# Kernel tuning notes

Hardware: AMD Instinct MI355X
Metric: run time of the kernel (lower is better)

The kernel has to match this reference:

```python
import jax, jax.numpy as jnp
import numpy as np

NUM_HEAD = 8


def setup_inputs() -> dict:
    key = jax.random.key(0)
    ks = jax.random.split(key, 9)
    B, T, Hz, N, H, Tc = 8, 48, 24, 1024, 512, 64
    return {
        "encoder_hidden": jax.random.normal(ks[0], (B, T, N, H), dtype=jnp.float32),
        "x_time": jax.random.normal(ks[1], (B, T, Tc), dtype=jnp.float32),
        "target_time": jax.random.normal(ks[2], (B, Hz, Tc), dtype=jnp.float32),
        "Wq": jax.random.normal(ks[3], (Tc, H), dtype=jnp.float32) * (Tc ** -0.5),
        "bq": jax.random.normal(ks[4], (H,), dtype=jnp.float32) * 0.02,
        "Wk": jax.random.normal(ks[5], (Tc, H), dtype=jnp.float32) * (Tc ** -0.5),
        "bk": jax.random.normal(ks[6], (H,), dtype=jnp.float32) * 0.02,
        "Wv": jax.random.normal(ks[7], (H, H), dtype=jnp.float32) * (H ** -0.5),
        "bv": jax.random.normal(ks[8], (H,), dtype=jnp.float32) * 0.02,
    }


def reference(encoder_hidden, x_time, target_time, Wq, bq, Wk, bk, Wv, bv):
    # encoder_hidden: [B, T, N, H]; x_time: [B, T, Tc]; target_time: [B, Hz, Tc]
    B, T, N, H = encoder_hidden.shape
    nh = NUM_HEAD
    d = H // nh
    Hz = target_time.shape[1]
    # Linear projections; split/cat over heads == reshape last dim to [nh, d]
    q = (target_time @ Wq + bq).reshape(B, Hz, nh, d)      # [B, Hz, nh, d]
    k = (x_time @ Wk + bk).reshape(B, T, nh, d)            # [B, T, nh, d]
    v = (encoder_hidden @ Wv + bv).reshape(B, T, N, nh, d)  # [B, T, N, nh, d]
    # Attention over time, shared across nodes
    scores = jnp.einsum('bihd,bjhd->bhij', q, k) / (d ** 0.5)  # [B, nh, Hz, T]
    attn = jax.nn.softmax(scores, axis=-1)
    # Broadcast attention across the node dimension
    X = jnp.einsum('bhij,bjnhd->binhd', attn, v)           # [B, Hz, N, nh, d]
    return X.reshape(B, Hz, N, H)                           # [B, Hz, N, H]
```

## Files before the change

### kernel.cpp

```cpp
#include <hip/hip_runtime.h>
#include <hip/hip_bf16.h>

#define Bb 8
#define Tt 48
#define HZ 24
#define Nn 1024
#define Hh 512
#define NHEAD 8

typedef short short8 __attribute__((ext_vector_type(8)));
typedef float f32x4 __attribute__((ext_vector_type(4)));

__device__ __forceinline__ ushort f2bf(float f) {
  uint u = __builtin_bit_cast(uint, f);
  u += 0x7FFFu + ((u >> 16) & 1u);
  return (ushort)(u >> 16);
}

__global__ void wvt2_kernel(const float* __restrict__ Wv, ushort* __restrict__ W2) {
  int t = blockIdx.x * 256 + threadIdx.x;
  int e = t & 7;
  int lane = (t >> 3) & 63;
  int f = (t >> 9) & 3;
  int kb = (t >> 11) & 7;
  int w = (t >> 14) & 3;
  int ch = t >> 16;
  int ki = f >> 1, nn = f & 1;
  int row = ch * 128 + w * 32 + nn * 16 + (lane & 15);
  int col = kb * 64 + ki * 32 + ((lane >> 4) << 3) + e;
  W2[t] = f2bf(Wv[col * 512 + row]);
}

__global__ void attn_kernel(const float* __restrict__ xt, const float* __restrict__ tt,
                            const float* __restrict__ Wq, const float* __restrict__ bq,
                            const float* __restrict__ Wk, const float* __restrict__ bk,
                            ushort* __restrict__ attnp) {
  __shared__ float qs[24][65];
  __shared__ float ks_[48][65];
  __shared__ float sc[24][49];
  int bh = blockIdx.x;
  int b = bh >> 3, h = bh & 7;
  int t = threadIdx.x;
  for (int e = t; e < 24 * 64; e += 256) {
    int i = e >> 6, dd = e & 63;
    float s = bq[h * 64 + dd];
    const float* r = tt + (b * 24 + i) * 64;
    #pragma unroll 8
    for (int c = 0; c < 64; ++c) s += r[c] * Wq[c * 512 + h * 64 + dd];
    qs[i][dd] = s;
  }
  for (int e = t; e < 48 * 64; e += 256) {
    int j = e >> 6, dd = e & 63;
    float s = bk[h * 64 + dd];
    const float* r = xt + (b * 48 + j) * 64;
    #pragma unroll 8
    for (int c = 0; c < 64; ++c) s += r[c] * Wk[c * 512 + h * 64 + dd];
    ks_[j][dd] = s;
  }
  __syncthreads();
  for (int e = t; e < 24 * 48; e += 256) {
    int i = e / 48, j = e - i * 48;
    float s = 0.f;
    #pragma unroll 8
    for (int dd = 0; dd < 64; ++dd) s += qs[i][dd] * ks_[j][dd];
    sc[i][j] = s * 0.125f;
  }
  __syncthreads();
  if (t < 32) {
    int i = t;
    ushort* orow = attnp + ((size_t)bh * 32 + i) * 64;
    if (i < 24) {
      float mx = -1e30f;
      for (int j = 0; j < 48; ++j) mx = fmaxf(mx, sc[i][j]);
      float sum = 0.f;
      for (int j = 0; j < 48; ++j) { float e = expf(sc[i][j] - mx); sc[i][j] = e; sum += e; }
      float inv = 1.f / sum;
      for (int j = 0; j < 48; ++j) orow[j] = f2bf(sc[i][j] * inv);
      for (int j = 48; j < 64; ++j) orow[j] = 0;
    } else {
      for (int j = 0; j < 64; ++j) orow[j] = 0;
    }
  }
}

#define A_BASE 0
#define V_BASE 49152

__global__ __launch_bounds__(256, 2) void main_kernel(
    const float* __restrict__ EH, const ushort* __restrict__ W2,
    const ushort* __restrict__ attnp, const float* __restrict__ bv,
    float* __restrict__ out) {
  __shared__ __align__(128) char smem[65536];
  int bid = blockIdx.x;
  int b = bid >> 10, n = bid & 1023;
  int t = threadIdx.x;
  int lane = t & 63, w = t >> 6;
  int rowl = lane & 15;
  int colb = (lane >> 4) << 3;
  char* vbuf = smem + V_BASE + w * 4096;

  float bvr[4][2];
  #pragma unroll
  for (int c = 0; c < 4; ++c)
    #pragma unroll
    for (int nn = 0; nn < 2; ++nn)
      bvr[c][nn] = bv[c * 128 + w * 32 + nn * 16 + rowl];

  {
    int lr = lane >> 1;
    int off = (lr << 7) + ((96 + ((lane & 1) << 4)) ^ ((lr & 7) << 4));
    *(uint4*)(vbuf + off) = make_uint4(0, 0, 0, 0);
  }

  const ushort* wp0 = W2 + (size_t)w * 16384 + lane * 8;

  short8 bc[4], bn[4];
  #pragma unroll
  for (int f = 0; f < 4; ++f) bc[f] = *(const short8*)(wp0 + f * 512);

  {
    const float* ehb = EH + (((size_t)b * Tt) * Nn + n) * Hh;
    #pragma unroll 8
    for (int it = 0; it < 24; ++it) {
      int f = it * 256 + t;
      int j = f >> 7, c4 = f & 127;
      float4 v = *(const float4*)(ehb + (size_t)j * (Nn * Hh) + c4 * 4);
      uint2 p;
      p.x = (uint)f2bf(v.x) | ((uint)f2bf(v.y) << 16);
      p.y = (uint)f2bf(v.z) | ((uint)f2bf(v.w) << 16);
      int off = (j << 10) + (c4 << 3);
      off ^= (j & 7) << 4;
      *(uint2*)(smem + A_BASE + off) = p;
    }
  }
  __syncthreads();

  #pragma unroll
  for (int ch = 0; ch < 4; ++ch) {
    const ushort* wp = W2 + (size_t)(ch * 4 + w) * 16384 + lane * 8;
    f32x4 acc[3][2] = {};
    #pragma unroll
    for (int kb = 0; kb < 8; ++kb) {
      if (kb < 7) {
        #pragma unroll
        for (int f = 0; f < 4; ++f)
          bn[f] = *(const short8*)(wp + (kb + 1) * 2048 + f * 512);
      } else if (ch < 3) {
        #pragma unroll
        for (int f = 0; f < 4; ++f)
          bn[f] = *(const short8*)(wp + 65536 + f * 512);
      }
      #pragma unroll
      for (int ki = 0; ki < 2; ++ki) {
        short8 af[3];
        int kc = kb * 64 + ki * 32 + colb;
        #pragma unroll
        for (int m = 0; m < 3; ++m) {
          int j = m * 16 + rowl;
          int off = (j << 10) + (kc << 1);
          off ^= (j & 7) << 4;
          af[m] = *(const short8*)(smem + A_BASE + off);
        }
        #pragma unroll
        for (int m = 0; m < 3; ++m) {
          acc[m][0] = __builtin_amdgcn_mfma_f32_16x16x32_bf16(af[m], bc[ki * 2 + 0], acc[m][0], 0, 0, 0);
          acc[m][1] = __builtin_amdgcn_mfma_f32_16x16x32_bf16(af[m], bc[ki * 2 + 1], acc[m][1], 0, 0, 0);
        }
      }
      #pragma unroll
      for (int f = 0; f < 4; ++f) bc[f] = bn[f];
    }

    int h = 2 * ch + (w >> 1);
    short8 pa[2][2];
    #pragma unroll
    for (int ks = 0; ks < 2; ++ks)
      #pragma unroll
      for (int itl = 0; itl < 2; ++itl) {
        int i = itl * 16 + rowl;
        pa[ks][itl] = *(const short8*)(attnp + (((size_t)(b * 8 + h) * 32 + i) * 64) + ks * 32 + colb);
      }

    #pragma unroll
    for (int m = 0; m < 3; ++m) {
      #pragma unroll
      for (int nn = 0; nn < 2; ++nn) {
        int lr = nn * 16 + rowl;
        int j0 = m * 16 + ((lane >> 4) << 2);
        uint2 p;
        p.x = (uint)f2bf(acc[m][nn][0]) | ((uint)f2bf(acc[m][nn][1]) << 16);
        p.y = (uint)f2bf(acc[m][nn][2]) | ((uint)f2bf(acc[m][nn][3]) << 16);
        int off = (lr << 7) + ((j0 << 1) ^ ((lr & 7) << 4));
        *(uint2*)(vbuf + off) = p;
      }
    }
    asm volatile("s_waitcnt lgkmcnt(0)" ::: "memory");
    __builtin_amdgcn_sched_barrier(0);

    f32x4 x[2][2] = {};
    #pragma unroll
    for (int ks = 0; ks < 2; ++ks) {
      short8 vb[2];
      #pragma unroll
      for (int nn = 0; nn < 2; ++nn) {
        int lr = nn * 16 + rowl;
        int off = (lr << 7) + (((ks * 32 + colb) << 1) ^ ((lr & 7) << 4));
        vb[nn] = *(const short8*)(vbuf + off);
      }
      #pragma unroll
      for (int itl = 0; itl < 2; ++itl)
        #pragma unroll
        for (int nn = 0; nn < 2; ++nn)
          x[itl][nn] = __builtin_amdgcn_mfma_f32_16x16x32_bf16(pa[ks][itl], vb[nn], x[itl][nn], 0, 0, 0);
    }

    #pragma unroll
    for (int itl = 0; itl < 2; ++itl) {
      int ib = itl * 16 + ((lane >> 4) << 2);
      #pragma unroll
      for (int nn = 0; nn < 2; ++nn) {
        int hd = ch * 128 + w * 32 + nn * 16 + rowl;
        float bvv = bvr[ch][nn];
        #pragma unroll
        for (int r = 0; r < 4; ++r) {
          int i = ib + r;
          if (i < 24)
            out[(((size_t)b * HZ + i) * Nn + n) * Hh + hd] = x[itl][nn][r] + bvv;
        }
      }
    }
  }
}

extern "C" void kernel_launch(void* const* d_in, const int* in_sizes, int n_in,
                              void* d_out, int out_size, void* d_ws, size_t ws_size,
                              hipStream_t stream) {
  (void)in_sizes; (void)n_in; (void)out_size; (void)ws_size;
  const float* EH = (const float*)d_in[0];
  const float* xt = (const float*)d_in[1];
  const float* tt = (const float*)d_in[2];
  const float* Wq = (const float*)d_in[3];
  const float* bq = (const float*)d_in[4];
  const float* Wk = (const float*)d_in[5];
  const float* bk = (const float*)d_in[6];
  const float* Wv = (const float*)d_in[7];
  const float* bv = (const float*)d_in[8];
  float* out = (float*)d_out;
  ushort* W2 = (ushort*)d_ws;
  ushort* attnp = (ushort*)((char*)d_ws + 512 * 1024);

  wvt2_kernel<<<1024, 256, 0, stream>>>(Wv, W2);
  attn_kernel<<<64, 256, 0, stream>>>(xt, tt, Wq, bq, Wk, bk, attnp);
  main_kernel<<<8192, 256, 0, stream>>>(EH, W2, attnp, bv, out);
}
```

Measured before the change: 468.9 us.

## Stream encoder tile in K chunks overlapped with MFMA, swap loop order

The kernel no longer loads the whole 48x512 encoder slice into shared memory before any compute. It loads two 64-wide K chunks up front, then inside a kb-outer loop it prefetches chunk kb+2 into registers, runs the MFMAs for all four output chunks on chunk kb, and converts and stores the prefetched chunk before a barrier. To make this possible the loop nest is inverted so all four ch accumulators live at once (96 floats per thread), and the Wv fragment prefetch is replaced by direct loads right before use. The aim is to hide global-memory latency behind matrix math. The cost is higher register pressure, a barrier per K step, and unprefetched weight loads.

```diff
diff --git a/kernel.cpp b/kernel.cpp
--- a/kernel.cpp
+++ b/kernel.cpp
@@ -112,65 +112,83 @@
     *(uint4*)(vbuf + off) = make_uint4(0, 0, 0, 0);
   }
 
-  const ushort* wp0 = W2 + (size_t)w * 16384 + lane * 8;
-
-  short8 bc[4], bn[4];
-  #pragma unroll
-  for (int f = 0; f < 4; ++f) bc[f] = *(const short8*)(wp0 + f * 512);
-
-  {
-    const float* ehb = EH + (((size_t)b * Tt) * Nn + n) * Hh;
-    #pragma unroll 8
-    for (int it = 0; it < 24; ++it) {
-      int f = it * 256 + t;
-      int j = f >> 7, c4 = f & 127;
-      float4 v = *(const float4*)(ehb + (size_t)j * (Nn * Hh) + c4 * 4);
+  const float* ehb = EH + (((size_t)b * Tt) * Nn + n) * Hh;
+  int sj = t >> 4, sc4 = t & 15;
+
+  #pragma unroll
+  for (int s = 0; s < 2; ++s) {
+    #pragma unroll
+    for (int i = 0; i < 3; ++i) {
+      int j = sj + i * 16;
+      float4 v = *(const float4*)(ehb + (size_t)j * (Nn * Hh) + (s * 16 + sc4) * 4);
       uint2 p;
       p.x = (uint)f2bf(v.x) | ((uint)f2bf(v.y) << 16);
       p.y = (uint)f2bf(v.z) | ((uint)f2bf(v.w) << 16);
-      int off = (j << 10) + (c4 << 3);
+      int off = (j << 10) + (((s * 16 + sc4)) << 3);
       off ^= (j & 7) << 4;
       *(uint2*)(smem + A_BASE + off) = p;
     }
   }
   __syncthreads();
 
+  f32x4 acc[4][3][2] = {};
+  #pragma unroll
+  for (int kb = 0; kb < 8; ++kb) {
+    float4 ldv[3];
+    if (kb < 6) {
+      #pragma unroll
+      for (int i = 0; i < 3; ++i) {
+        int j = sj + i * 16;
+        ldv[i] = *(const float4*)(ehb + (size_t)j * (Nn * Hh) + ((kb + 2) * 16 + sc4) * 4);
+      }
+    }
+    short8 af[2][3];
+    #pragma unroll
+    for (int ki = 0; ki < 2; ++ki) {
+      int kc = kb * 64 + ki * 32 + colb;
+      #pragma unroll
+      for (int m = 0; m < 3; ++m) {
+        int j = m * 16 + rowl;
+        int off = (j << 10) + (kc << 1);
+        off ^= (j & 7) << 4;
+        af[ki][m] = *(const short8*)(smem + A_BASE + off);
+      }
+    }
+    #pragma unroll
+    for (int ch = 0; ch < 4; ++ch) {
+      const ushort* wpf = W2 + (size_t)(ch * 4 + w) * 16384 + kb * 2048 + lane * 8;
+      short8 bf0 = *(const short8*)(wpf);
+      short8 bf1 = *(const short8*)(wpf + 512);
+      short8 bf2 = *(const short8*)(wpf + 1024);
+      short8 bf3 = *(const short8*)(wpf + 1536);
+      #pragma unroll
+      for (int m = 0; m < 3; ++m) {
+        acc[ch][m][0] = __builtin_amdgcn_mfma_f32_16x16x32_bf16(af[0][m], bf0, acc[ch][m][0], 0, 0, 0);
+        acc[ch][m][1] = __builtin_amdgcn_mfma_f32_16x16x32_bf16(af[0][m], bf1, acc[ch][m][1], 0, 0, 0);
+      }
+      #pragma unroll
+      for (int m = 0; m < 3; ++m) {
+        acc[ch][m][0] = __builtin_amdgcn_mfma_f32_16x16x32_bf16(af[1][m], bf2, acc[ch][m][0], 0, 0, 0);
+        acc[ch][m][1] = __builtin_amdgcn_mfma_f32_16x16x32_bf16(af[1][m], bf3, acc[ch][m][1], 0, 0, 0);
+      }
+    }
+    if (kb < 6) {
+      #pragma unroll
+      for (int i = 0; i < 3; ++i) {
+        int j = sj + i * 16;
+        uint2 p;
+        p.x = (uint)f2bf(ldv[i].x) | ((uint)f2bf(ldv[i].y) << 16);
+        p.y = (uint)f2bf(ldv[i].z) | ((uint)f2bf(ldv[i].w) << 16);
+        int off = (j << 10) + (((kb + 2) * 16 + sc4)) << 3;
+        off = ((j << 10) + (((kb + 2) * 16 + sc4) << 3)) ^ ((j & 7) << 4);
+        *(uint2*)(smem + A_BASE + off) = p;
+      }
+    }
+    __syncthreads();
+  }
+
   #pragma unroll
   for (int ch = 0; ch < 4; ++ch) {
-    const ushort* wp = W2 + (size_t)(ch * 4 + w) * 16384 + lane * 8;
-    f32x4 acc[3][2] = {};
-    #pragma unroll
-    for (int kb = 0; kb < 8; ++kb) {
-      if (kb < 7) {
-        #pragma unroll
-        for (int f = 0; f < 4; ++f)
-          bn[f] = *(const short8*)(wp + (kb + 1) * 2048 + f * 512);
-      } else if (ch < 3) {
-        #pragma unroll
-        for (int f = 0; f < 4; ++f)
-          bn[f] = *(const short8*)(wp + 65536 + f * 512);
-      }
-      #pragma unroll
-      for (int ki = 0; ki < 2; ++ki) {
-        short8 af[3];
-        int kc = kb * 64 + ki * 32 + colb;
-        #pragma unroll
-        for (int m = 0; m < 3; ++m) {
-          int j = m * 16 + rowl;
-          int off = (j << 10) + (kc << 1);
-          off ^= (j & 7) << 4;
-          af[m] = *(const short8*)(smem + A_BASE + off);
-        }
-        #pragma unroll
-        for (int m = 0; m < 3; ++m) {
-          acc[m][0] = __builtin_amdgcn_mfma_f32_16x16x32_bf16(af[m], bc[ki * 2 + 0], acc[m][0], 0, 0, 0);
-          acc[m][1] = __builtin_amdgcn_mfma_f32_16x16x32_bf16(af[m], bc[ki * 2 + 1], acc[m][1], 0, 0, 0);
-        }
-      }
-      #pragma unroll
-      for (int f = 0; f < 4; ++f) bc[f] = bn[f];
-    }
-
     int h = 2 * ch + (w >> 1);
     short8 pa[2][2];
     #pragma unroll
@@ -188,8 +206,8 @@
         int lr = nn * 16 + rowl;
         int j0 = m * 16 + ((lane >> 4) << 2);
         uint2 p;
-        p.x = (uint)f2bf(acc[m][nn][0]) | ((uint)f2bf(acc[m][nn][1]) << 16);
-        p.y = (uint)f2bf(acc[m][nn][2]) | ((uint)f2bf(acc[m][nn][3]) << 16);
+        p.x = (uint)f2bf(acc[ch][m][nn][0]) | ((uint)f2bf(acc[ch][m][nn][1]) << 16);
+        p.y = (uint)f2bf(acc[ch][m][nn][2]) | ((uint)f2bf(acc[ch][m][nn][3]) << 16);
         int off = (lr << 7) + ((j0 << 1) ^ ((lr & 7) << 4));
         *(uint2*)(vbuf + off) = p;
       }
@@ -213,6 +231,8 @@
         for (int nn = 0; nn < 2; ++nn)
           x[itl][nn] = __builtin_amdgcn_mfma_f32_16x16x32_bf16(pa[ks][itl], vb[nn], x[itl][nn], 0, 0, 0);
     }
+    asm volatile("s_waitcnt lgkmcnt(0)" ::: "memory");
+    __builtin_amdgcn_sched_barrier(0);
 
     #pragma unroll
     for (int itl = 0; itl < 2; ++itl) {
```

Result: slower. 531.5 us (+13.3%).

## Feed V accumulators directly into 16x16x16 MFMA, drop LDS staging

Applied to the files above, without the earlier changes.

The V-projection accumulators are converted to bf16 in registers and used directly as the B operand of 16x16x16 bf16 MFMAs for the attention product. The per-wave LDS round-trip buffer and its waitcnt barrier are removed. This shrinks shared memory from 64KB to 48KB so launch bounds can allow 3 blocks per CU instead of 2. In exchange it issues more, smaller MFMAs and makes more narrow global loads of the attention weights.

```diff
diff --git a/kernel.cpp b/kernel.cpp
--- a/kernel.cpp
+++ b/kernel.cpp
@@ -9,12 +9,26 @@
 #define NHEAD 8
 
 typedef short short8 __attribute__((ext_vector_type(8)));
+typedef short bf16x4 __attribute__((ext_vector_type(4)));
 typedef float f32x4 __attribute__((ext_vector_type(4)));
 
 __device__ __forceinline__ ushort f2bf(float f) {
   uint u = __builtin_bit_cast(uint, f);
   u += 0x7FFFu + ((u >> 16) & 1u);
   return (ushort)(u >> 16);
+}
+
+__device__ __forceinline__ f32x4 mfma16(bf16x4 a, bf16x4 b, f32x4 c) {
+#if __has_builtin(__builtin_amdgcn_mfma_f32_16x16x16bf16_1k)
+  return __builtin_amdgcn_mfma_f32_16x16x16bf16_1k(a, b, c, 0, 0, 0);
+#elif __has_builtin(__builtin_amdgcn_mfma_f32_16x16x16_bf16)
+  return __builtin_amdgcn_mfma_f32_16x16x16_bf16(a, b, c, 0, 0, 0);
+#else
+  f32x4 d;
+  asm volatile("v_mfma_f32_16x16x16_bf16 %0, %1, %2, %3\n\ts_nop 7\n\ts_nop 4"
+               : "=v"(d) : "v"(a), "v"(b), "v"(c));
+  return d;
+#endif
 }
 
 __global__ void wvt2_kernel(const float* __restrict__ Wv, ushort* __restrict__ W2) {
@@ -84,20 +98,19 @@
 }
 
 #define A_BASE 0
-#define V_BASE 49152
-
-__global__ __launch_bounds__(256, 2) void main_kernel(
+
+__global__ __launch_bounds__(256, 3) void main_kernel(
     const float* __restrict__ EH, const ushort* __restrict__ W2,
     const ushort* __restrict__ attnp, const float* __restrict__ bv,
     float* __restrict__ out) {
-  __shared__ __align__(128) char smem[65536];
+  __shared__ __align__(128) char smem[49152];
   int bid = blockIdx.x;
   int b = bid >> 10, n = bid & 1023;
   int t = threadIdx.x;
   int lane = t & 63, w = t >> 6;
   int rowl = lane & 15;
   int colb = (lane >> 4) << 3;
-  char* vbuf = smem + V_BASE + w * 4096;
+  int colb16 = (lane >> 4) << 2;
 
   float bvr[4][2];
   #pragma unroll
@@ -105,12 +118,6 @@
     #pragma unroll
     for (int nn = 0; nn < 2; ++nn)
       bvr[c][nn] = bv[c * 128 + w * 32 + nn * 16 + rowl];
-
-  {
-    int lr = lane >> 1;
-    int off = (lr << 7) + ((96 + ((lane & 1) << 4)) ^ ((lr & 7) << 4));
-    *(uint4*)(vbuf + off) = make_uint4(0, 0, 0, 0);
-  }
 
   const ushort* wp0 = W2 + (size_t)w * 16384 + lane * 8;
 
@@ -172,46 +179,24 @@
     }
 
     int h = 2 * ch + (w >> 1);
-    short8 pa[2][2];
-    #pragma unroll
-    for (int ks = 0; ks < 2; ++ks)
-      #pragma unroll
-      for (int itl = 0; itl < 2; ++itl) {
-        int i = itl * 16 + rowl;
-        pa[ks][itl] = *(const short8*)(attnp + (((size_t)(b * 8 + h) * 32 + i) * 64) + ks * 32 + colb);
-      }
-
+    const ushort* arow = attnp + ((size_t)(b * 8 + h) * 32) * 64;
+    f32x4 x[2][2] = {};
     #pragma unroll
     for (int m = 0; m < 3; ++m) {
+      bf16x4 pa[2];
+      #pragma unroll
+      for (int itl = 0; itl < 2; ++itl)
+        pa[itl] = *(const bf16x4*)(arow + (itl * 16 + rowl) * 64 + m * 16 + colb16);
       #pragma unroll
       for (int nn = 0; nn < 2; ++nn) {
-        int lr = nn * 16 + rowl;
-        int j0 = m * 16 + ((lane >> 4) << 2);
-        uint2 p;
-        p.x = (uint)f2bf(acc[m][nn][0]) | ((uint)f2bf(acc[m][nn][1]) << 16);
-        p.y = (uint)f2bf(acc[m][nn][2]) | ((uint)f2bf(acc[m][nn][3]) << 16);
-        int off = (lr << 7) + ((j0 << 1) ^ ((lr & 7) << 4));
-        *(uint2*)(vbuf + off) = p;
-      }
-    }
-    asm volatile("s_waitcnt lgkmcnt(0)" ::: "memory");
-    __builtin_amdgcn_sched_barrier(0);
-
-    f32x4 x[2][2] = {};
-    #pragma unroll
-    for (int ks = 0; ks < 2; ++ks) {
-      short8 vb[2];
-      #pragma unroll
-      for (int nn = 0; nn < 2; ++nn) {
-        int lr = nn * 16 + rowl;
-        int off = (lr << 7) + (((ks * 32 + colb) << 1) ^ ((lr & 7) << 4));
-        vb[nn] = *(const short8*)(vbuf + off);
-      }
-      #pragma unroll
-      for (int itl = 0; itl < 2; ++itl)
-        #pragma unroll
-        for (int nn = 0; nn < 2; ++nn)
-          x[itl][nn] = __builtin_amdgcn_mfma_f32_16x16x32_bf16(pa[ks][itl], vb[nn], x[itl][nn], 0, 0, 0);
+        bf16x4 vbq;
+        vbq[0] = (short)f2bf(acc[m][nn][0]);
+        vbq[1] = (short)f2bf(acc[m][nn][1]);
+        vbq[2] = (short)f2bf(acc[m][nn][2]);
+        vbq[3] = (short)f2bf(acc[m][nn][3]);
+        x[0][nn] = mfma16(pa[0], vbq, x[0][nn]);
+        x[1][nn] = mfma16(pa[1], vbq, x[1][nn]);
+      }
     }
 
     #pragma unroll
```

After: 484.5 us. 3.3% more time.
